# Performance work log

Hardware: AMD Instinct MI355X
Metric: run time of the kernel (lower is better)

Reference implementation:

```python
import jax, jax.numpy as jnp
import numpy as np

DIM = 3
N_FEATURES = 4
FEATURE_TABLE_SIZE = 1048576   # 2^20 (power of 2: uint32 hash math matches torch int64 exactly)
INDEX_TABLE_SIZE = 524288      # 2^19
N_LEARNABLE = 8
RESOLUTION = 128.0
N_POINTS = 500000
PRIMES = np.array([1, 2654435761, 805459861, 3674653429, 2097192037, 1434869437, 2165219737], dtype=np.uint32)

# corner mask [2^dim, dim]: True where the corner uses floor(x) on that axis
_neigs = np.arange(1 << DIM, dtype=np.int64)[:, None]
_dims = np.arange(DIM, dtype=np.int64)[None, :]
BIN_MASK = jnp.asarray((_neigs & (1 << _dims)) == 0)


def setup_inputs() -> dict:
    key = jax.random.key(0)
    k1, k2, k3 = jax.random.split(key, 3)
    x = jax.random.uniform(k1, (N_POINTS, DIM), dtype=jnp.float32)
    feature_table = jax.random.uniform(k2, (FEATURE_TABLE_SIZE, N_FEATURES), dtype=jnp.float32,
                                       minval=-1e-4, maxval=1e-4)
    index_table = jax.random.normal(k3, (INDEX_TABLE_SIZE, N_LEARNABLE), dtype=jnp.float32)
    return {"x": x, "feature_table": feature_table, "index_table": index_table}


def _fast_hash(inds):
    # inds: [N, 2^dim, dim] int32 (nonnegative). tiny-cuda-nn fast hash in uint32
    u = inds.astype(jnp.uint32) * jnp.asarray(PRIMES[:DIM])
    h = u[..., 0]
    for i in range(1, DIM):
        h = h ^ u[..., i]
    return h % jnp.uint32(INDEX_TABLE_SIZE)  # uint32 [N, 2^dim]


def reference(x, feature_table, index_table):
    softmax_t = 1.0
    xs = x * RESOLUTION                                   # [N, dim]
    xi = xs.astype(jnp.int32)                             # trunc == floor for x >= 0
    xf = xs - jax.lax.stop_gradient(xi.astype(xs.dtype))  # fractional part, grads flow through xs
    xi = xi[:, None, :]                                   # [N, 1, dim]
    xf = xf[:, None, :]
    inds = jnp.where(BIN_MASK, xi, xi + 1)                # [N, 2^dim, dim]
    ws = jnp.where(BIN_MASK, 1.0 - xf, xf)
    w = jnp.prod(ws, axis=-1, keepdims=True)              # trilinear weights [N, 2^dim, 1]

    hash_ids = _fast_hash(inds)                           # uint32 [N, 2^dim]
    feature_weights = index_table[hash_ids.astype(jnp.int32)]  # [N, 2^dim, L]

    # second (index->feature-table) hash; power-of-2 modulus makes uint32 exact
    ar = jnp.arange(N_LEARNABLE, dtype=jnp.uint32)[None, None, :]
    a = (ar * jnp.uint32(PRIMES[1])) ^ (hash_ids[:, :, None] * jnp.uint32(PRIMES[2]))
    a = (a % jnp.uint32(FEATURE_TABLE_SIZE)).astype(jnp.int32)   # [N, 2^dim, L]

    features = feature_table[a]                                  # [N, 2^dim, L, F]
    fw = jax.nn.softmax(feature_weights * softmax_t, axis=-1)    # [N, 2^dim, L]
    features = jnp.sum(features * fw[..., None], axis=-2)        # [N, 2^dim, F]
    out = jnp.sum(features * w, axis=-2)                         # [N, F]
    return out
```

## Files before the change

### kernel.cpp

```cpp
#include <hip/hip_runtime.h>

#define NPOINTS 500000
#define RESOLUTION 128.0f
#define IDX_SIZE 524288u
#define IDX_MASK 0x7FFFFu
#define FEAT_MASK 0xFFFFFu
#define P1 2654435761u
#define P2 805459861u

typedef float    f4v __attribute__((ext_vector_type(4)));
typedef unsigned u2v __attribute__((ext_vector_type(2)));

constexpr unsigned mulinv32(unsigned a) {
    unsigned x = 1u;
    for (int i = 0; i < 6; ++i) x *= 2u - a * x;
    return x;
}
constexpr unsigned P2INV = mulinv32(P2);
static_assert(((P2INV * P2) & FEAT_MASK) == 1u, "bad inverse");

__device__ inline unsigned bf16pack(float a, float b) {
    unsigned ua = __float_as_uint(a); ua = (ua + 0x7FFFu + ((ua >> 16) & 1u)) >> 16;
    unsigned ub = __float_as_uint(b); ub = (ub + 0x7FFFu + ((ub >> 16) & 1u)) >> 16;
    return ua | (ub << 16);
}

__global__ __launch_bounds__(256) void build_F_y(
    const f4v* __restrict__ ftp,
    const float* __restrict__ index_table,
    u2v* __restrict__ F)
{
    unsigned y = blockIdx.x * blockDim.x + threadIdx.x;
    unsigned h = (y * P2INV) & FEAT_MASK;
    bool valid = h < IDX_SIZE;

    f4v fv[8];
#pragma unroll
    for (unsigned j = 0; j < 8; ++j) {
        unsigned cj = (j * P1) & FEAT_MASK;
        fv[j] = ftp[y ^ cj];
    }

    if (!valid) return;

    const f4v* p = (const f4v*)(index_table + (size_t)h * 8u);
    f4v iw0 = p[0];
    f4v iw1 = p[1];
    float e[8] = { iw0.x, iw0.y, iw0.z, iw0.w, iw1.x, iw1.y, iw1.z, iw1.w };

    float mx = fmaxf(fmaxf(fmaxf(e[0], e[1]), fmaxf(e[2], e[3])),
                     fmaxf(fmaxf(e[4], e[5]), fmaxf(e[6], e[7])));
    float s = 0.f;
#pragma unroll
    for (int j = 0; j < 8; ++j) { e[j] = __expf(e[j] - mx); s += e[j]; }

    float ax = 0.f, ay = 0.f, az = 0.f, aw = 0.f;
#pragma unroll
    for (int j = 0; j < 8; ++j) {
        ax = fmaf(fv[j].x, e[j], ax);
        ay = fmaf(fv[j].y, e[j], ay);
        az = fmaf(fv[j].z, e[j], az);
        aw = fmaf(fv[j].w, e[j], aw);
    }
    float inv = 1.0f / s;
    ax *= inv; ay *= inv; az *= inv; aw *= inv;

    u2v packed;
    packed.x = bf16pack(ax, ay);
    packed.y = bf16pack(az, aw);
    F[h] = packed;
}

__global__ __launch_bounds__(256) void interp(
    const float* __restrict__ x,
    const u2v* __restrict__ F,
    float4* __restrict__ out)
{
    int p = blockIdx.x * blockDim.x + threadIdx.x;
    if (p >= NPOINTS) return;

    float xs0 = x[p * 3 + 0] * RESOLUTION;
    float xs1 = x[p * 3 + 1] * RESOLUTION;
    float xs2 = x[p * 3 + 2] * RESOLUTION;
    int i0 = (int)xs0, i1 = (int)xs1, i2 = (int)xs2;
    float f0 = xs0 - (float)i0, f1 = xs1 - (float)i1, f2 = xs2 - (float)i2;
    float g0 = 1.0f - f0, g1 = 1.0f - f1, g2 = 1.0f - f2;

    unsigned u0 = (unsigned)i0;
    unsigned m1a = (unsigned)i1 * P1, m1b = ((unsigned)i1 + 1u) * P1;
    unsigned m2a = (unsigned)i2 * P2, m2b = ((unsigned)i2 + 1u) * P2;

    float ax = 0.f, ay = 0.f, az = 0.f, aw = 0.f;
#pragma unroll
    for (int c = 0; c < 8; ++c) {
        unsigned b0 = c & 1, b1 = (c >> 1) & 1, b2 = (c >> 2) & 1;
        unsigned h = ((u0 + b0) ^ (b1 ? m1b : m1a) ^ (b2 ? m2b : m2a)) & IDX_MASK;
        float w = (b0 ? f0 : g0) * (b1 ? f1 : g1) * (b2 ? f2 : g2);
        u2v fv = F[h];
        float fx = __uint_as_float(fv.x << 16);
        float fy = __uint_as_float(fv.x & 0xFFFF0000u);
        float fz = __uint_as_float(fv.y << 16);
        float fw = __uint_as_float(fv.y & 0xFFFF0000u);
        ax = fmaf(fx, w, ax);
        ay = fmaf(fy, w, ay);
        az = fmaf(fz, w, az);
        aw = fmaf(fw, w, aw);
    }
    out[p] = make_float4(ax, ay, az, aw);
}

__global__ __launch_bounds__(256) void hashgrid_fwd(
    const float* __restrict__ x,
    const float* __restrict__ feature_table,
    const float* __restrict__ index_table,
    float* __restrict__ out)
{
    int tid = blockIdx.x * blockDim.x + threadIdx.x;
    int p = tid >> 3;
    int corner = tid & 7;
    if (p >= NPOINTS) return;

    float xs0 = x[p * 3 + 0] * RESOLUTION;
    float xs1 = x[p * 3 + 1] * RESOLUTION;
    float xs2 = x[p * 3 + 2] * RESOLUTION;
    int i0 = (int)xs0, i1 = (int)xs1, i2 = (int)xs2;
    float f0 = xs0 - (float)i0, f1 = xs1 - (float)i1, f2 = xs2 - (float)i2;

    unsigned b0 = corner & 1u, b1 = (corner >> 1) & 1u, b2 = (corner >> 2) & 1u;
    unsigned ind0 = (unsigned)i0 + b0;
    unsigned ind1 = (unsigned)i1 + b1;
    unsigned ind2 = (unsigned)i2 + b2;
    float w0 = b0 ? f0 : 1.0f - f0;
    float w1 = b1 ? f1 : 1.0f - f1;
    float w2 = b2 ? f2 : 1.0f - f2;
    float w = w0 * w1 * w2;

    unsigned h = (ind0 ^ ind1 * P1 ^ ind2 * P2) & IDX_MASK;

    const float4* itp = (const float4*)(index_table + (size_t)h * 8u);
    float4 iw0 = itp[0];
    float4 iw1 = itp[1];
    float e0 = iw0.x, e1 = iw0.y, e2 = iw0.z, e3 = iw0.w;
    float e4 = iw1.x, e5 = iw1.y, e6 = iw1.z, e7 = iw1.w;

    float mx = fmaxf(fmaxf(fmaxf(e0, e1), fmaxf(e2, e3)),
                     fmaxf(fmaxf(e4, e5), fmaxf(e6, e7)));
    e0 = __expf(e0 - mx); e1 = __expf(e1 - mx);
    e2 = __expf(e2 - mx); e3 = __expf(e3 - mx);
    e4 = __expf(e4 - mx); e5 = __expf(e5 - mx);
    e6 = __expf(e6 - mx); e7 = __expf(e7 - mx);
    float s = ((e0 + e1) + (e2 + e3)) + ((e4 + e5) + (e6 + e7));

    unsigned hp2 = h * P2;
    const float4* ftp = (const float4*)feature_table;
    float ax = 0.f, ay = 0.f, az = 0.f, aw = 0.f;
    float ej[8] = {e0, e1, e2, e3, e4, e5, e6, e7};
#pragma unroll
    for (unsigned j = 0; j < 8; ++j) {
        unsigned a = ((j * P1) ^ hp2) & FEAT_MASK;
        float4 ft = ftp[a];
        ax = fmaf(ft.x, ej[j], ax);
        ay = fmaf(ft.y, ej[j], ay);
        az = fmaf(ft.z, ej[j], az);
        aw = fmaf(ft.w, ej[j], aw);
    }

    float scale = w / s;
    ax *= scale; ay *= scale; az *= scale; aw *= scale;

#pragma unroll
    for (int m = 1; m < 8; m <<= 1) {
        ax += __shfl_xor(ax, m);
        ay += __shfl_xor(ay, m);
        az += __shfl_xor(az, m);
        aw += __shfl_xor(aw, m);
    }
    if (corner == 0) {
        ((float4*)out)[p] = make_float4(ax, ay, az, aw);
    }
}

extern "C" void kernel_launch(void* const* d_in, const int* in_sizes, int n_in,
                              void* d_out, int out_size, void* d_ws, size_t ws_size,
                              hipStream_t stream) {
    const float* x  = (const float*)d_in[0];
    const float* ft = (const float*)d_in[1];
    const float* it = (const float*)d_in[2];

    const size_t F_BYTES = (size_t)IDX_SIZE * 8u;

    if (ws_size >= F_BYTES) {
        u2v* F = (u2v*)d_ws;
        hipLaunchKernelGGL(build_F_y, dim3((1u << 20) / 256), dim3(256), 0, stream,
                           (const f4v*)ft, it, F);
        const int grid2 = (NPOINTS + 255) / 256;
        hipLaunchKernelGGL(interp, dim3(grid2), dim3(256), 0, stream,
                           x, F, (float4*)d_out);
    } else {
        const int total = NPOINTS * 8;
        hipLaunchKernelGGL(hashgrid_fwd, dim3((total + 255) / 256), dim3(256), 0, stream,
                           x, ft, it, (float*)d_out);
    }
}
```

Baseline: 58.12 us.

## Split softmax into separate scatter pass and parallelize interpolation per corner

Adds a softmax pre-pass that computes normalized index-table weights, packs them as fp16 and scatters them into y-order, so the F-building pass reads them with coalesced loads instead of gathering index-table rows. Interpolation now uses one thread per corner with shuffle reductions instead of one thread per point looping over eight corners, which raises parallelism for the gathers. The cost is an extra kernel launch, 16 MB of additional workspace traffic and fp16 rounding of the weights, with a fallback to the old path when workspace is small.

```diff
diff --git a/kernel.cpp b/kernel.cpp
--- a/kernel.cpp
+++ b/kernel.cpp
@@ -1,4 +1,5 @@
 #include <hip/hip_runtime.h>
+#include <hip/hip_fp16.h>
 
 #define NPOINTS 500000
 #define RESOLUTION 128.0f
@@ -10,6 +11,7 @@
 
 typedef float    f4v __attribute__((ext_vector_type(4)));
 typedef unsigned u2v __attribute__((ext_vector_type(2)));
+typedef unsigned u4v __attribute__((ext_vector_type(4)));
 
 constexpr unsigned mulinv32(unsigned a) {
     unsigned x = 1u;
@@ -25,6 +27,84 @@
     return ua | (ub << 16);
 }
 
+__device__ inline unsigned f16pack(float a, float b) {
+    __half2 h = __floats2half2_rn(a, b);
+    union { __half2 h; unsigned u; } cv; cv.h = h;
+    return cv.u;
+}
+__device__ inline float f16lo(unsigned u) {
+    union { unsigned u; __half2 h; } cv; cv.u = u;
+    return __low2float(cv.h);
+}
+__device__ inline float f16hi(unsigned u) {
+    union { unsigned u; __half2 h; } cv; cv.u = u;
+    return __high2float(cv.h);
+}
+
+__global__ __launch_bounds__(256) void softmax_E(
+    const float* __restrict__ index_table,
+    u4v* __restrict__ E)
+{
+    unsigned h = blockIdx.x * blockDim.x + threadIdx.x;
+
+    const f4v* p = (const f4v*)(index_table + (size_t)h * 8u);
+    f4v iw0 = p[0];
+    f4v iw1 = p[1];
+    float e[8] = { iw0.x, iw0.y, iw0.z, iw0.w, iw1.x, iw1.y, iw1.z, iw1.w };
+
+    float mx = fmaxf(fmaxf(fmaxf(e[0], e[1]), fmaxf(e[2], e[3])),
+                     fmaxf(fmaxf(e[4], e[5]), fmaxf(e[6], e[7])));
+    float s = 0.f;
+#pragma unroll
+    for (int j = 0; j < 8; ++j) { e[j] = __expf(e[j] - mx); s += e[j]; }
+    float inv = 1.0f / s;
+
+    u4v ev;
+    ev.x = f16pack(e[0] * inv, e[1] * inv);
+    ev.y = f16pack(e[2] * inv, e[3] * inv);
+    ev.z = f16pack(e[4] * inv, e[5] * inv);
+    ev.w = f16pack(e[6] * inv, e[7] * inv);
+
+    unsigned y = (h * P2) & FEAT_MASK;
+    __builtin_nontemporal_store(ev, E + y);
+}
+
+__global__ __launch_bounds__(256) void build_F_from_E(
+    const f4v* __restrict__ ftp,
+    const u4v* __restrict__ E,
+    u2v* __restrict__ F)
+{
+    unsigned y = blockIdx.x * blockDim.x + threadIdx.x;
+    unsigned h = (y * P2INV) & FEAT_MASK;
+    if (h >= IDX_SIZE) return;
+
+    u4v ev = E[y];
+
+    f4v fv[8];
+#pragma unroll
+    for (unsigned j = 0; j < 8; ++j) {
+        unsigned cj = (j * P1) & FEAT_MASK;
+        fv[j] = ftp[y ^ cj];
+    }
+
+    float q[8] = { f16lo(ev.x), f16hi(ev.x), f16lo(ev.y), f16hi(ev.y),
+                   f16lo(ev.z), f16hi(ev.z), f16lo(ev.w), f16hi(ev.w) };
+
+    float ax = 0.f, ay = 0.f, az = 0.f, aw = 0.f;
+#pragma unroll
+    for (int j = 0; j < 8; ++j) {
+        ax = fmaf(fv[j].x, q[j], ax);
+        ay = fmaf(fv[j].y, q[j], ay);
+        az = fmaf(fv[j].z, q[j], az);
+        aw = fmaf(fv[j].w, q[j], aw);
+    }
+
+    u2v packed;
+    packed.x = bf16pack(ax, ay);
+    packed.y = bf16pack(az, aw);
+    __builtin_nontemporal_store(packed, F + h);
+}
+
 __global__ __launch_bounds__(256) void build_F_y(
     const f4v* __restrict__ ftp,
     const float* __restrict__ index_table,
@@ -32,7 +112,11 @@
 {
     unsigned y = blockIdx.x * blockDim.x + threadIdx.x;
     unsigned h = (y * P2INV) & FEAT_MASK;
-    bool valid = h < IDX_SIZE;
+    if (h >= IDX_SIZE) return;
+
+    const f4v* p = (const f4v*)(index_table + (size_t)h * 8u);
+    f4v iw0 = p[0];
+    f4v iw1 = p[1];
 
     f4v fv[8];
 #pragma unroll
@@ -41,13 +125,7 @@
         fv[j] = ftp[y ^ cj];
     }
 
-    if (!valid) return;
-
-    const f4v* p = (const f4v*)(index_table + (size_t)h * 8u);
-    f4v iw0 = p[0];
-    f4v iw1 = p[1];
     float e[8] = { iw0.x, iw0.y, iw0.z, iw0.w, iw1.x, iw1.y, iw1.z, iw1.w };
-
     float mx = fmaxf(fmaxf(fmaxf(e[0], e[1]), fmaxf(e[2], e[3])),
                      fmaxf(fmaxf(e[4], e[5]), fmaxf(e[6], e[7])));
     float s = 0.f;
@@ -63,50 +141,49 @@
         aw = fmaf(fv[j].w, e[j], aw);
     }
     float inv = 1.0f / s;
-    ax *= inv; ay *= inv; az *= inv; aw *= inv;
-
     u2v packed;
-    packed.x = bf16pack(ax, ay);
-    packed.y = bf16pack(az, aw);
+    packed.x = bf16pack(ax * inv, ay * inv);
+    packed.y = bf16pack(az * inv, aw * inv);
     F[h] = packed;
 }
 
-__global__ __launch_bounds__(256) void interp(
+__global__ __launch_bounds__(256) void interp_corner(
     const float* __restrict__ x,
     const u2v* __restrict__ F,
-    float4* __restrict__ out)
-{
-    int p = blockIdx.x * blockDim.x + threadIdx.x;
-    if (p >= NPOINTS) return;
+    f4v* __restrict__ out)
+{
+    int tid = blockIdx.x * blockDim.x + threadIdx.x;
+    int p = tid >> 3;
+    int corner = tid & 7;
 
     float xs0 = x[p * 3 + 0] * RESOLUTION;
     float xs1 = x[p * 3 + 1] * RESOLUTION;
     float xs2 = x[p * 3 + 2] * RESOLUTION;
     int i0 = (int)xs0, i1 = (int)xs1, i2 = (int)xs2;
     float f0 = xs0 - (float)i0, f1 = xs1 - (float)i1, f2 = xs2 - (float)i2;
-    float g0 = 1.0f - f0, g1 = 1.0f - f1, g2 = 1.0f - f2;
-
-    unsigned u0 = (unsigned)i0;
-    unsigned m1a = (unsigned)i1 * P1, m1b = ((unsigned)i1 + 1u) * P1;
-    unsigned m2a = (unsigned)i2 * P2, m2b = ((unsigned)i2 + 1u) * P2;
-
-    float ax = 0.f, ay = 0.f, az = 0.f, aw = 0.f;
-#pragma unroll
-    for (int c = 0; c < 8; ++c) {
-        unsigned b0 = c & 1, b1 = (c >> 1) & 1, b2 = (c >> 2) & 1;
-        unsigned h = ((u0 + b0) ^ (b1 ? m1b : m1a) ^ (b2 ? m2b : m2a)) & IDX_MASK;
-        float w = (b0 ? f0 : g0) * (b1 ? f1 : g1) * (b2 ? f2 : g2);
-        u2v fv = F[h];
-        float fx = __uint_as_float(fv.x << 16);
-        float fy = __uint_as_float(fv.x & 0xFFFF0000u);
-        float fz = __uint_as_float(fv.y << 16);
-        float fw = __uint_as_float(fv.y & 0xFFFF0000u);
-        ax = fmaf(fx, w, ax);
-        ay = fmaf(fy, w, ay);
-        az = fmaf(fz, w, az);
-        aw = fmaf(fw, w, aw);
-    }
-    out[p] = make_float4(ax, ay, az, aw);
+
+    unsigned b0 = corner & 1u, b1 = (corner >> 1) & 1u, b2 = (corner >> 2) & 1u;
+    unsigned h = (((unsigned)i0 + b0) ^ (((unsigned)i1 + b1) * P1)
+                  ^ (((unsigned)i2 + b2) * P2)) & IDX_MASK;
+    float w = (b0 ? f0 : 1.0f - f0) * (b1 ? f1 : 1.0f - f1) * (b2 ? f2 : 1.0f - f2);
+
+    u2v fv = F[h];
+    float ax = __uint_as_float(fv.x << 16) * w;
+    float ay = __uint_as_float(fv.x & 0xFFFF0000u) * w;
+    float az = __uint_as_float(fv.y << 16) * w;
+    float aw = __uint_as_float(fv.y & 0xFFFF0000u) * w;
+
+#pragma unroll
+    for (int m = 1; m < 8; m <<= 1) {
+        ax += __shfl_xor(ax, m);
+        ay += __shfl_xor(ay, m);
+        az += __shfl_xor(az, m);
+        aw += __shfl_xor(aw, m);
+    }
+    if (corner == 0) {
+        f4v o = { ax, ay, az, aw };
+        out[p] = o;
+    }
 }
 
 __global__ __launch_bounds__(256) void hashgrid_fwd(
@@ -127,15 +204,13 @@
     float f0 = xs0 - (float)i0, f1 = xs1 - (float)i1, f2 = xs2 - (float)i2;
 
     unsigned b0 = corner & 1u, b1 = (corner >> 1) & 1u, b2 = (corner >> 2) & 1u;
-    unsigned ind0 = (unsigned)i0 + b0;
-    unsigned ind1 = (unsigned)i1 + b1;
-    unsigned ind2 = (unsigned)i2 + b2;
     float w0 = b0 ? f0 : 1.0f - f0;
     float w1 = b1 ? f1 : 1.0f - f1;
     float w2 = b2 ? f2 : 1.0f - f2;
     float w = w0 * w1 * w2;
 
-    unsigned h = (ind0 ^ ind1 * P1 ^ ind2 * P2) & IDX_MASK;
+    unsigned h = (((unsigned)i0 + b0) ^ (((unsigned)i1 + b1) * P1)
+                  ^ (((unsigned)i2 + b2) * P2)) & IDX_MASK;
 
     const float4* itp = (const float4*)(index_table + (size_t)h * 8u);
     float4 iw0 = itp[0];
@@ -188,14 +263,23 @@
     const float* it = (const float*)d_in[2];
 
     const size_t F_BYTES = (size_t)IDX_SIZE * 8u;
-
-    if (ws_size >= F_BYTES) {
+    const size_t E_BYTES = (size_t)(1u << 20) * 16u;
+
+    if (ws_size >= F_BYTES + E_BYTES) {
+        u2v* F = (u2v*)d_ws;
+        u4v* E = (u4v*)((char*)d_ws + F_BYTES);
+        hipLaunchKernelGGL(softmax_E, dim3(IDX_SIZE / 256), dim3(256), 0, stream,
+                           it, E);
+        hipLaunchKernelGGL(build_F_from_E, dim3((1u << 20) / 256), dim3(256), 0, stream,
+                           (const f4v*)ft, E, F);
+        hipLaunchKernelGGL(interp_corner, dim3(NPOINTS * 8 / 256), dim3(256), 0, stream,
+                           x, F, (f4v*)d_out);
+    } else if (ws_size >= F_BYTES) {
         u2v* F = (u2v*)d_ws;
         hipLaunchKernelGGL(build_F_y, dim3((1u << 20) / 256), dim3(256), 0, stream,
                            (const f4v*)ft, it, F);
-        const int grid2 = (NPOINTS + 255) / 256;
-        hipLaunchKernelGGL(interp, dim3(grid2), dim3(256), 0, stream,
-                           x, F, (float4*)d_out);
+        hipLaunchKernelGGL(interp_corner, dim3(NPOINTS * 8 / 256), dim3(256), 0, stream,
+                           x, F, (f4v*)d_out);
     } else {
         const int total = NPOINTS * 8;
         hipLaunchKernelGGL(hashgrid_fwd, dim3((total + 255) / 256), dim3(256), 0, stream,
```

Measured after the change: 63.18 us. 8.7% more time.
